# Kernel tuning notes

Measured on AMD Instinct MI355X. Metric: run time of the kernel, lower is better.

The kernel has to match this reference:

```python
import jax, jax.numpy as jnp
import numpy as np

N_QUBITS = 10
N_LAYERS = 4
NUM_CLASSES = 10
BATCH = 2048
DIM = 1 << N_QUBITS  # 1024 state-vector dimension

# basis-state bit tables (wire w <-> bit position w; any consistent ordering
# yields identical PauliZ expectation values)
_d = np.arange(DIM)
_bits = (_d[None, :] >> np.arange(N_QUBITS)[:, None]) & 1          # [n, D]
_SIGN = jnp.asarray(1.0 - 2.0 * _bits, dtype=jnp.float32)         # [n, D], z_w(d) = +/-1
_ZZ = _SIGN[:-1] * _SIGN[1:]                                       # [n-1, D], z_i*z_{i+1}
# CNOT(control=i, target=i+1) basis permutations (self-inverse)
_CNOT_PERM = [np.where((_d >> i) & 1, _d ^ (1 << (i + 1)), _d) for i in range(N_QUBITS - 1)]


def _apply_ry(state, theta, wire):
    # state: [B, D] complex64, theta: scalar angle, RY = [[c,-s],[s,c]], c=cos(theta/2)
    B, D = state.shape
    lo = 1 << wire
    st = state.reshape(B, D // (2 * lo), 2, lo)
    c = jnp.cos(0.5 * theta)
    s = jnp.sin(0.5 * theta)
    s0, s1 = st[:, :, 0, :], st[:, :, 1, :]
    return jnp.stack([c * s0 - s * s1, s * s0 + c * s1], axis=2).reshape(B, D)


def _circuit(inp, weights):
    # inp: [B, n] rotation angles (pre_net output), weights: [L+1, n]
    B = inp.shape[0]
    # Hadamards on |0...0> -> uniform superposition
    state = jnp.full((B, DIM), DIM ** -0.5, dtype=jnp.complex64)
    # ZZFeatureMap is fully diagonal: RZ(2*x_i) gives phase exp(-1j*x_i*z_i);
    # CNOT-RZ(2*(pi-x_i)*(pi-x_{i+1}))-CNOT gives phase exp(-1j*(pi-x_i)*(pi-x_{i+1})*z_i*z_{i+1})
    ang = inp @ _SIGN + ((np.pi - inp[:, :-1]) * (np.pi - inp[:, 1:])) @ _ZZ  # [B, D]
    state = state * jnp.exp(-1j * ang)
    # RealAmplitudes-style ansatz
    for l in range(N_LAYERS):
        for i in range(N_QUBITS):
            state = _apply_ry(state, weights[l, i], i)
        for p in _CNOT_PERM:
            state = state[:, p]
    for i in range(N_QUBITS):
        state = _apply_ry(state, weights[N_LAYERS, i], i)
    probs = jnp.square(state.real) + jnp.square(state.imag)  # [B, D]
    return probs @ _SIGN.T                                    # [B, n] PauliZ expvals


def setup_inputs() -> dict:
    k = jax.random.split(jax.random.key(0), 5)
    x = jax.random.normal(k[0], (BATCH, N_QUBITS), jnp.float32)
    W_pre = jax.random.normal(k[1], (N_QUBITS, N_QUBITS), jnp.float32) / np.sqrt(N_QUBITS).astype(np.float32)
    b_pre = jnp.zeros((N_QUBITS,), jnp.float32)
    # TorchLayer default init: uniform(0, 2*pi)
    weights = jax.random.uniform(k[2], (N_LAYERS + 1, N_QUBITS), jnp.float32, 0.0, 2.0 * np.pi)
    W_post = jax.random.normal(k[3], (NUM_CLASSES, N_QUBITS), jnp.float32) / np.sqrt(N_QUBITS).astype(np.float32)
    b_post = jnp.zeros((NUM_CLASSES,), jnp.float32)
    return {"x": x, "W_pre": W_pre, "b_pre": b_pre, "weights": weights,
            "W_post": W_post, "b_post": b_post}


def reference(x, W_pre, b_pre, weights, W_post, b_post):
    h = x @ W_pre.T + b_pre          # pre_net
    q = _circuit(h, weights)         # qlayer: batched state-vector simulation
    return q @ W_post.T + b_post     # post_net
```

## Files before the change

kernel.cpp:

```cpp
#include <hip/hip_runtime.h>

#define NQ   10
#define NL   4
#define NCL  10
#define PI_F 3.14159265358979f

typedef float f2 __attribute__((ext_vector_type(2)));

__device__ __forceinline__ f2 pk_mul2(f2 a, f2 b) {
    f2 d;
    asm("v_pk_mul_f32 %0, %1, %2" : "=v"(d) : "v"(a), "v"(b));
    return d;
}
__device__ __forceinline__ f2 pk_fma2(f2 a, f2 b, f2 c) {
    f2 d;
    asm("v_pk_fma_f32 %0, %1, %2, %3" : "=v"(d) : "v"(a), "v"(b), "v"(c));
    return d;
}
__device__ __forceinline__ f2 pk_add2(f2 a, f2 b) {
    f2 d;
    asm("v_pk_add_f32 %0, %1, %2" : "=v"(d) : "v"(a), "v"(b));
    return d;
}

__device__ __forceinline__ float bcastf(float v, int l) {
    return __int_as_float(__builtin_amdgcn_readlane(__float_as_int(v), l));
}

__device__ __forceinline__ float bperm(int byteaddr, float v) {
    return __int_as_float(__builtin_amdgcn_ds_bpermute(byteaddr, __float_as_int(v)));
}

template<int M>
__device__ __forceinline__ float xlane(float v) {
    if constexpr (M == 1) {
        return __int_as_float(__builtin_amdgcn_update_dpp(
            __float_as_int(v), __float_as_int(v), 0xB1, 0xF, 0xF, false));
    } else if constexpr (M == 2) {
        return __int_as_float(__builtin_amdgcn_update_dpp(
            __float_as_int(v), __float_as_int(v), 0x4E, 0xF, 0xF, false));
    } else if constexpr (M == 4) {
        return __int_as_float(__builtin_amdgcn_ds_swizzle(
            __float_as_int(v), 0x101F));
    } else if constexpr (M == 8) {
        return __int_as_float(__builtin_amdgcn_update_dpp(
            __float_as_int(v), __float_as_int(v), 0x128, 0xF, 0xF, false));
    } else if constexpr (M == 16) {
        auto r = __builtin_amdgcn_permlane16_swap(
            (unsigned)__float_as_int(v), (unsigned)__float_as_int(v), false, false);
        return __int_as_float((int)(r[0] ^ r[1] ^ (unsigned)__float_as_int(v)));
    } else {
        auto r = __builtin_amdgcn_permlane32_swap(
            (unsigned)__float_as_int(v), (unsigned)__float_as_int(v), false, false);
        return __int_as_float((int)(r[0] ^ r[1] ^ (unsigned)__float_as_int(v)));
    }
}

template<int M>
__device__ __forceinline__ f2 xlane2(f2 v) {
    f2 r; r.x = xlane<M>(v.x); r.y = xlane<M>(v.y); return r;
}

template<int M>
__device__ __forceinline__ void xwire2(float c, float s, int lane, f2 (&sc)[16]) {
    const float se = (lane & M) ? s : -s;
    const f2 c2 = {c, c}, se2 = {se, se};
    #pragma unroll
    for (int r = 0; r < 16; ++r) {
        f2 t = xlane2<M>(sc[r]);
        sc[r] = pk_fma2(se2, t, pk_mul2(c2, sc[r]));
    }
}

__device__ __forceinline__ f2 bsum2(f2 v) {
    v = pk_add2(v, xlane2<1 >(v));
    v = pk_add2(v, xlane2<2 >(v));
    v = pk_add2(v, xlane2<4 >(v));
    v = pk_add2(v, xlane2<8 >(v));
    v = pk_add2(v, xlane2<16>(v));
    v = pk_add2(v, xlane2<32>(v));
    return v;
}

__global__ __launch_bounds__(256)
void qnn_kernel(const float* __restrict__ x,
                const float* __restrict__ W_pre,
                const float* __restrict__ b_pre,
                const float* __restrict__ weights,
                const float* __restrict__ W_post,
                const float* __restrict__ b_post,
                float* __restrict__ out, int batch)
{
    const int lane = threadIdx.x & 63;
    const int b = blockIdx.x * 4 + (threadIdx.x >> 6);
    if (b >= batch) return;
    const int bu = __builtin_amdgcn_readfirstlane(b);

    float cw = 0.0f, sw = 0.0f;
    if (lane < (NL + 1) * NQ) {
        float th = 0.5f * weights[lane];
        __sincosf(th, &sw, &cw);
    }

    float xv[NQ];
    #pragma unroll
    for (int k = 0; k < NQ; ++k) xv[k] = x[bu * NQ + k];
    float h[NQ];
    #pragma unroll
    for (int j = 0; j < NQ; ++j) {
        float acc = b_pre[j];
        #pragma unroll
        for (int k = 0; k < NQ; ++k)
            acc = fmaf(xv[k], W_pre[j * NQ + k], acc);
        h[j] = acc;
    }
    float z[NQ - 1];
    #pragma unroll
    for (int i = 0; i < NQ - 1; ++i) z[i] = (PI_F - h[i]) * (PI_F - h[i + 1]);

    float A = 0.0f;
    #pragma unroll
    for (int i = 4; i < NQ; ++i)
        A += ((lane >> (i - 4)) & 1) ? -h[i] : h[i];
    #pragma unroll
    for (int i = 4; i < NQ - 1; ++i)
        A += (((lane >> (i - 4)) ^ (lane >> (i - 3))) & 1) ? -z[i] : z[i];

    f2 sc[16];
    #pragma unroll
    for (int r = 0; r < 16; ++r) {
        float ang = A;
        #pragma unroll
        for (int i = 0; i < 4; ++i)
            ang += ((r >> i) & 1) ? -h[i] : h[i];
        #pragma unroll
        for (int i = 0; i < 3; ++i)
            ang += (((r >> i) ^ (r >> (i + 1))) & 1) ? -z[i] : z[i];
        ang += (((r >> 3) ^ lane) & 1) ? -z[3] : z[3];
        float sn, cn;
        __sincosf(ang, &sn, &cn);
        sc[r].x = 0.03125f * cn;
        sc[r].y = -0.03125f * sn;
    }

    const int plbase = (lane ^ (lane << 1)) & 0x3F;
    const int paddr0 = plbase << 2;
    const int paddr1 = (plbase ^ 1) << 2;

    #pragma clang loop unroll(disable)
    for (int l = 0; l <= NL; ++l) {
        if (l > 0) {
            f2 np[16];
            #pragma unroll
            for (int r = 0; r < 16; ++r) {
                const int rp = (r ^ (r << 1)) & 0xF;
                const int pa = (r < 8) ? paddr0 : paddr1;
                np[r].x = bperm(pa, sc[rp].x);
                np[r].y = bperm(pa, sc[rp].y);
            }
            #pragma unroll
            for (int r = 0; r < 16; ++r) sc[r] = np[r];
        }

        const int base = l * NQ;

        #pragma unroll
        for (int w = 0; w < 4; ++w) {
            const float c = bcastf(cw, base + w);
            const float s = bcastf(sw, base + w);
            const f2 c2 = {c, c}, s2 = {s, s}, ns2 = {-s, -s};
            #pragma unroll
            for (int r = 0; r < 16; ++r) {
                if (r & (1 << w)) continue;
                const int q = r | (1 << w);
                f2 a0 = sc[r], a1 = sc[q];
                sc[r] = pk_fma2(ns2, a1, pk_mul2(c2, a0));
                sc[q] = pk_fma2(s2,  a0, pk_mul2(c2, a1));
            }
        }

        xwire2<1 >(bcastf(cw, base + 4), bcastf(sw, base + 4), lane, sc);
        xwire2<2 >(bcastf(cw, base + 5), bcastf(sw, base + 5), lane, sc);
        xwire2<4 >(bcastf(cw, base + 6), bcastf(sw, base + 6), lane, sc);
        xwire2<8 >(bcastf(cw, base + 7), bcastf(sw, base + 7), lane, sc);
        xwire2<16>(bcastf(cw, base + 8), bcastf(sw, base + 8), lane, sc);
        xwire2<32>(bcastf(cw, base + 9), bcastf(sw, base + 9), lane, sc);
    }

    float P = 0.0f, p0 = 0.0f, p1 = 0.0f, p2 = 0.0f, p3 = 0.0f;
    #pragma unroll
    for (int r = 0; r < 16; ++r) {
        f2 qq = pk_mul2(sc[r], sc[r]);
        float pr = qq.x + qq.y;
        P  += pr;
        p0 += (r & 1) ? -pr : pr;
        p1 += (r & 2) ? -pr : pr;
        p2 += (r & 4) ? -pr : pr;
        p3 += (r & 8) ? -pr : pr;
    }
    f2 qa = bsum2((f2){p0, p1});
    f2 qb = bsum2((f2){p2, p3});
    {
        float t;
        t = xlane<1 >(P); P = t + ((lane & 1 ) ? -P : P);
        t = xlane<2 >(P); P = t + ((lane & 2 ) ? -P : P);
        t = xlane<4 >(P); P = t + ((lane & 4 ) ? -P : P);
        t = xlane<8 >(P); P = t + ((lane & 8 ) ? -P : P);
        t = xlane<16>(P); P = t + ((lane & 16) ? -P : P);
        t = xlane<32>(P); P = t + ((lane & 32) ? -P : P);
    }
    float q[NCL];
    q[0] = qa.x; q[1] = qa.y; q[2] = qb.x; q[3] = qb.y;
    q[4] = bcastf(P, 1);
    q[5] = bcastf(P, 2);
    q[6] = bcastf(P, 4);
    q[7] = bcastf(P, 8);
    q[8] = bcastf(P, 16);
    q[9] = bcastf(P, 32);

    if (lane < NCL) {
        float o = b_post[lane];
        #pragma unroll
        for (int k = 0; k < NCL; ++k)
            o = fmaf(q[k], W_post[lane * NQ + k], o);
        out[b * NCL + lane] = o;
    }
}

extern "C" void kernel_launch(void* const* d_in, const int* in_sizes, int n_in,
                              void* d_out, int out_size, void* d_ws, size_t ws_size,
                              hipStream_t stream) {
    const float* x       = (const float*)d_in[0];
    const float* W_pre   = (const float*)d_in[1];
    const float* b_pre   = (const float*)d_in[2];
    const float* weights = (const float*)d_in[3];
    const float* W_post  = (const float*)d_in[4];
    const float* b_post  = (const float*)d_in[5];
    float* outp = (float*)d_out;
    int batch = in_sizes[0] / NQ;
    int grid = (batch + 3) / 4;
    qnn_kernel<<<grid, 256, 0, stream>>>(x, W_pre, b_pre, weights, W_post, b_post, outp, batch);
}
```

Baseline: 28.14 us.

## Split each sample's state vector across two wavefronts with LDS exchange for wire 0

Each batch sample is now simulated by a 128-thread block of two wavefronts. Each wave holds 8 amplitude pairs per lane instead of 16, with wire 0 mapped to the wave index. The wire-0 rotation exchanges halves through double-buffered shared memory with a block barrier each layer, and the final expectation values are combined across the two waves in LDS. The aim is to halve per-thread register state and double wave-level parallelism, in exchange for LDS traffic and five extra barriers per sample.

```diff
diff --git a/kernel.cpp b/kernel.cpp
--- a/kernel.cpp
+++ b/kernel.cpp
@@ -8,25 +8,18 @@
 typedef float f2 __attribute__((ext_vector_type(2)));
 
 __device__ __forceinline__ f2 pk_mul2(f2 a, f2 b) {
-    f2 d;
-    asm("v_pk_mul_f32 %0, %1, %2" : "=v"(d) : "v"(a), "v"(b));
-    return d;
+    f2 d; asm("v_pk_mul_f32 %0, %1, %2" : "=v"(d) : "v"(a), "v"(b)); return d;
 }
 __device__ __forceinline__ f2 pk_fma2(f2 a, f2 b, f2 c) {
-    f2 d;
-    asm("v_pk_fma_f32 %0, %1, %2, %3" : "=v"(d) : "v"(a), "v"(b), "v"(c));
-    return d;
+    f2 d; asm("v_pk_fma_f32 %0, %1, %2, %3" : "=v"(d) : "v"(a), "v"(b), "v"(c)); return d;
 }
 __device__ __forceinline__ f2 pk_add2(f2 a, f2 b) {
-    f2 d;
-    asm("v_pk_add_f32 %0, %1, %2" : "=v"(d) : "v"(a), "v"(b));
-    return d;
+    f2 d; asm("v_pk_add_f32 %0, %1, %2" : "=v"(d) : "v"(a), "v"(b)); return d;
 }
 
 __device__ __forceinline__ float bcastf(float v, int l) {
     return __int_as_float(__builtin_amdgcn_readlane(__float_as_int(v), l));
 }
-
 __device__ __forceinline__ float bperm(int byteaddr, float v) {
     return __int_as_float(__builtin_amdgcn_ds_bpermute(byteaddr, __float_as_int(v)));
 }
@@ -55,21 +48,20 @@
         return __int_as_float((int)(r[0] ^ r[1] ^ (unsigned)__float_as_int(v)));
     }
 }
-
 template<int M>
 __device__ __forceinline__ f2 xlane2(f2 v) {
     f2 r; r.x = xlane<M>(v.x); r.y = xlane<M>(v.y); return r;
 }
 
 template<int M>
-__device__ __forceinline__ void xwire2(float c, float s, int lane, f2 (&sc)[16]) {
+__device__ __forceinline__ void xwire8(float c, float s, int lane, f2 (&sc)[8]) {
     const float se = (lane & M) ? s : -s;
     const f2 c2 = {c, c}, se2 = {se, se};
-    #pragma unroll
-    for (int r = 0; r < 16; ++r) {
-        f2 t = xlane2<M>(sc[r]);
-        sc[r] = pk_fma2(se2, t, pk_mul2(c2, sc[r]));
-    }
+    f2 t[8];
+    #pragma unroll
+    for (int r = 0; r < 8; ++r) t[r] = xlane2<M>(sc[r]);
+    #pragma unroll
+    for (int r = 0; r < 8; ++r) sc[r] = pk_fma2(se2, t[r], pk_mul2(c2, sc[r]));
 }
 
 __device__ __forceinline__ f2 bsum2(f2 v) {
@@ -82,7 +74,7 @@
     return v;
 }
 
-__global__ __launch_bounds__(256)
+__global__ __launch_bounds__(128, 4)
 void qnn_kernel(const float* __restrict__ x,
                 const float* __restrict__ W_pre,
                 const float* __restrict__ b_pre,
@@ -91,10 +83,13 @@
                 const float* __restrict__ b_post,
                 float* __restrict__ out, int batch)
 {
-    const int lane = threadIdx.x & 63;
-    const int b = blockIdx.x * 4 + (threadIdx.x >> 6);
-    if (b >= batch) return;
-    const int bu = __builtin_amdgcn_readfirstlane(b);
+    __shared__ f2 xch[2][2][8][64];
+    __shared__ float sq[2][NCL];
+
+    const int tid  = threadIdx.x;
+    const int lane = tid & 63;
+    const int W    = tid >> 6;
+    const int b    = blockIdx.x;
 
     float cw = 0.0f, sw = 0.0f;
     if (lane < (NL + 1) * NQ) {
@@ -104,7 +99,7 @@
 
     float xv[NQ];
     #pragma unroll
-    for (int k = 0; k < NQ; ++k) xv[k] = x[bu * NQ + k];
+    for (int k = 0; k < NQ; ++k) xv[k] = x[b * NQ + k];
     float h[NQ];
     #pragma unroll
     for (int j = 0; j < NQ; ++j) {
@@ -118,59 +113,72 @@
     #pragma unroll
     for (int i = 0; i < NQ - 1; ++i) z[i] = (PI_F - h[i]) * (PI_F - h[i + 1]);
 
-    float A = 0.0f;
-    #pragma unroll
-    for (int i = 4; i < NQ; ++i)
-        A += ((lane >> (i - 4)) & 1) ? -h[i] : h[i];
-    #pragma unroll
-    for (int i = 4; i < NQ - 1; ++i)
-        A += (((lane >> (i - 4)) ^ (lane >> (i - 3))) & 1) ? -z[i] : z[i];
-
-    f2 sc[16];
-    #pragma unroll
-    for (int r = 0; r < 16; ++r) {
+    float A = W ? -h[0] : h[0];
+    #pragma unroll
+    for (int i = 0; i < 6; ++i)
+        A += ((lane >> i) & 1) ? -h[4 + i] : h[4 + i];
+    #pragma unroll
+    for (int j = 0; j < 5; ++j)
+        A += (((lane >> j) ^ (lane >> (j + 1))) & 1) ? -z[4 + j] : z[4 + j];
+    const float zw0 = W ? -z[0] : z[0];
+    const float zl3 = (lane & 1) ? -z[3] : z[3];
+
+    f2 sc[8];
+    #pragma unroll
+    for (int r = 0; r < 8; ++r) {
         float ang = A;
-        #pragma unroll
-        for (int i = 0; i < 4; ++i)
-            ang += ((r >> i) & 1) ? -h[i] : h[i];
-        #pragma unroll
-        for (int i = 0; i < 3; ++i)
-            ang += (((r >> i) ^ (r >> (i + 1))) & 1) ? -z[i] : z[i];
-        ang += (((r >> 3) ^ lane) & 1) ? -z[3] : z[3];
+        ang += (r & 1) ? -h[1] : h[1];
+        ang += (r & 2) ? -h[2] : h[2];
+        ang += (r & 4) ? -h[3] : h[3];
+        ang += (r & 1) ? -zw0 : zw0;
+        ang += ((r ^ (r >> 1)) & 1) ? -z[1] : z[1];
+        ang += (((r >> 1) ^ (r >> 2)) & 1) ? -z[2] : z[2];
+        ang += (r & 4) ? -zl3 : zl3;
         float sn, cn;
         __sincosf(ang, &sn, &cn);
         sc[r].x = 0.03125f * cn;
         sc[r].y = -0.03125f * sn;
     }
 
-    const int plbase = (lane ^ (lane << 1)) & 0x3F;
-    const int paddr0 = plbase << 2;
-    const int paddr1 = (plbase ^ 1) << 2;
+    const int plb = (lane ^ (lane << 1)) & 0x3F;
+    const int pa0 = plb << 2;
+    const int pa1 = (plb ^ 1) << 2;
+    int pp = 0;
 
     #pragma clang loop unroll(disable)
     for (int l = 0; l <= NL; ++l) {
         if (l > 0) {
-            f2 np[16];
-            #pragma unroll
-            for (int r = 0; r < 16; ++r) {
-                const int rp = (r ^ (r << 1)) & 0xF;
-                const int pa = (r < 8) ? paddr0 : paddr1;
-                np[r].x = bperm(pa, sc[rp].x);
-                np[r].y = bperm(pa, sc[rp].y);
+            f2 np[8];
+            if (W == 0) {
+                #pragma unroll
+                for (int r = 0; r < 8; ++r) {
+                    const int rp = (r ^ (r << 1)) & 7;
+                    const int pa = (r < 4) ? pa0 : pa1;
+                    np[r].x = bperm(pa, sc[rp].x);
+                    np[r].y = bperm(pa, sc[rp].y);
+                }
+            } else {
+                #pragma unroll
+                for (int r = 0; r < 8; ++r) {
+                    const int rp = ((r ^ (r << 1)) & 7) ^ 1;
+                    const int pa = (r < 4) ? pa0 : pa1;
+                    np[r].x = bperm(pa, sc[rp].x);
+                    np[r].y = bperm(pa, sc[rp].y);
+                }
             }
             #pragma unroll
-            for (int r = 0; r < 16; ++r) sc[r] = np[r];
+            for (int r = 0; r < 8; ++r) sc[r] = np[r];
         }
 
         const int base = l * NQ;
 
         #pragma unroll
-        for (int w = 0; w < 4; ++w) {
-            const float c = bcastf(cw, base + w);
-            const float s = bcastf(sw, base + w);
+        for (int w = 0; w < 3; ++w) {
+            const float c = bcastf(cw, base + 1 + w);
+            const float s = bcastf(sw, base + 1 + w);
             const f2 c2 = {c, c}, s2 = {s, s}, ns2 = {-s, -s};
             #pragma unroll
-            for (int r = 0; r < 16; ++r) {
+            for (int r = 0; r < 8; ++r) {
                 if (r & (1 << w)) continue;
                 const int q = r | (1 << w);
                 f2 a0 = sc[r], a1 = sc[q];
@@ -179,27 +187,42 @@
             }
         }
 
-        xwire2<1 >(bcastf(cw, base + 4), bcastf(sw, base + 4), lane, sc);
-        xwire2<2 >(bcastf(cw, base + 5), bcastf(sw, base + 5), lane, sc);
-        xwire2<4 >(bcastf(cw, base + 6), bcastf(sw, base + 6), lane, sc);
-        xwire2<8 >(bcastf(cw, base + 7), bcastf(sw, base + 7), lane, sc);
-        xwire2<16>(bcastf(cw, base + 8), bcastf(sw, base + 8), lane, sc);
-        xwire2<32>(bcastf(cw, base + 9), bcastf(sw, base + 9), lane, sc);
-    }
-
-    float P = 0.0f, p0 = 0.0f, p1 = 0.0f, p2 = 0.0f, p3 = 0.0f;
-    #pragma unroll
-    for (int r = 0; r < 16; ++r) {
+        xwire8<1 >(bcastf(cw, base + 4), bcastf(sw, base + 4), lane, sc);
+        xwire8<2 >(bcastf(cw, base + 5), bcastf(sw, base + 5), lane, sc);
+        xwire8<4 >(bcastf(cw, base + 6), bcastf(sw, base + 6), lane, sc);
+        xwire8<8 >(bcastf(cw, base + 7), bcastf(sw, base + 7), lane, sc);
+        xwire8<16>(bcastf(cw, base + 8), bcastf(sw, base + 8), lane, sc);
+        xwire8<32>(bcastf(cw, base + 9), bcastf(sw, base + 9), lane, sc);
+
+        {
+            const float c = bcastf(cw, base + 0);
+            const float s = bcastf(sw, base + 0);
+            #pragma unroll
+            for (int r = 0; r < 8; ++r) xch[pp][W][r][lane] = sc[r];
+            __syncthreads();
+            const float se = W ? s : -s;
+            const f2 c2 = {c, c}, se2 = {se, se};
+            #pragma unroll
+            for (int r = 0; r < 8; ++r) {
+                f2 t = xch[pp][W ^ 1][r][lane];
+                sc[r] = pk_fma2(se2, t, pk_mul2(c2, sc[r]));
+            }
+            pp ^= 1;
+        }
+    }
+
+    float P = 0.0f, p0 = 0.0f, p1 = 0.0f, p2 = 0.0f;
+    #pragma unroll
+    for (int r = 0; r < 8; ++r) {
         f2 qq = pk_mul2(sc[r], sc[r]);
         float pr = qq.x + qq.y;
         P  += pr;
         p0 += (r & 1) ? -pr : pr;
         p1 += (r & 2) ? -pr : pr;
         p2 += (r & 4) ? -pr : pr;
-        p3 += (r & 8) ? -pr : pr;
     }
     f2 qa = bsum2((f2){p0, p1});
-    f2 qb = bsum2((f2){p2, p3});
+    f2 qb = bsum2((f2){p2, p2});
     {
         float t;
         t = xlane<1 >(P); P = t + ((lane & 1 ) ? -P : P);
@@ -209,20 +232,23 @@
         t = xlane<16>(P); P = t + ((lane & 16) ? -P : P);
         t = xlane<32>(P); P = t + ((lane & 32) ? -P : P);
     }
-    float q[NCL];
-    q[0] = qa.x; q[1] = qa.y; q[2] = qb.x; q[3] = qb.y;
-    q[4] = bcastf(P, 1);
-    q[5] = bcastf(P, 2);
-    q[6] = bcastf(P, 4);
-    q[7] = bcastf(P, 8);
-    q[8] = bcastf(P, 16);
-    q[9] = bcastf(P, 32);
-
-    if (lane < NCL) {
+    const float T  = bcastf(P, 0);
+    const float s4 = bcastf(P, 1),  s5 = bcastf(P, 2),  s6 = bcastf(P, 4);
+    const float s7 = bcastf(P, 8),  s8 = bcastf(P, 16), s9 = bcastf(P, 32);
+
+    if (lane == 0) {
+        sq[W][0] = W ? -T : T;
+        sq[W][1] = qa.x; sq[W][2] = qa.y; sq[W][3] = qb.x;
+        sq[W][4] = s4; sq[W][5] = s5; sq[W][6] = s6;
+        sq[W][7] = s7; sq[W][8] = s8; sq[W][9] = s9;
+    }
+    __syncthreads();
+
+    if (W == 0 && lane < NCL) {
         float o = b_post[lane];
         #pragma unroll
         for (int k = 0; k < NCL; ++k)
-            o = fmaf(q[k], W_post[lane * NQ + k], o);
+            o = fmaf(sq[0][k] + sq[1][k], W_post[lane * NQ + k], o);
         out[b * NCL + lane] = o;
     }
 }
@@ -238,6 +264,5 @@
     const float* b_post  = (const float*)d_in[5];
     float* outp = (float*)d_out;
     int batch = in_sizes[0] / NQ;
-    int grid = (batch + 3) / 4;
-    qnn_kernel<<<grid, 256, 0, stream>>>(x, W_pre, b_pre, weights, W_post, b_post, outp, batch);
-}
+    qnn_kernel<<<batch, 128, 0, stream>>>(x, W_pre, b_pre, weights, W_post, b_post, outp, batch);
+}
```

Measured after the change: 30.34 us. 7.8% more time.

## Launch one wavefront per block and batch cross-lane swaps before FMAs

Applied to the files above, without the earlier changes.

Switches the launch to one 64-thread block per sample instead of four wavefronts per 256-thread block, and drops the bounds check and readfirstlane. Restructures the cross-lane wire updates so all 16 lane exchanges are issued before the FMAs, which exposes more independent exchanges to hide their latency but raises register pressure. Replaces the XOR trick that extracts the partner value from permlane swaps with a compare-and-select.

```diff
diff --git a/kernel.cpp b/kernel.cpp
--- a/kernel.cpp
+++ b/kernel.cpp
@@ -8,25 +8,18 @@
 typedef float f2 __attribute__((ext_vector_type(2)));
 
 __device__ __forceinline__ f2 pk_mul2(f2 a, f2 b) {
-    f2 d;
-    asm("v_pk_mul_f32 %0, %1, %2" : "=v"(d) : "v"(a), "v"(b));
-    return d;
+    f2 d; asm("v_pk_mul_f32 %0, %1, %2" : "=v"(d) : "v"(a), "v"(b)); return d;
 }
 __device__ __forceinline__ f2 pk_fma2(f2 a, f2 b, f2 c) {
-    f2 d;
-    asm("v_pk_fma_f32 %0, %1, %2, %3" : "=v"(d) : "v"(a), "v"(b), "v"(c));
-    return d;
+    f2 d; asm("v_pk_fma_f32 %0, %1, %2, %3" : "=v"(d) : "v"(a), "v"(b), "v"(c)); return d;
 }
 __device__ __forceinline__ f2 pk_add2(f2 a, f2 b) {
-    f2 d;
-    asm("v_pk_add_f32 %0, %1, %2" : "=v"(d) : "v"(a), "v"(b));
-    return d;
+    f2 d; asm("v_pk_add_f32 %0, %1, %2" : "=v"(d) : "v"(a), "v"(b)); return d;
 }
 
 __device__ __forceinline__ float bcastf(float v, int l) {
     return __int_as_float(__builtin_amdgcn_readlane(__float_as_int(v), l));
 }
-
 __device__ __forceinline__ float bperm(int byteaddr, float v) {
     return __int_as_float(__builtin_amdgcn_ds_bpermute(byteaddr, __float_as_int(v)));
 }
@@ -46,16 +39,17 @@
         return __int_as_float(__builtin_amdgcn_update_dpp(
             __float_as_int(v), __float_as_int(v), 0x128, 0xF, 0xF, false));
     } else if constexpr (M == 16) {
-        auto r = __builtin_amdgcn_permlane16_swap(
-            (unsigned)__float_as_int(v), (unsigned)__float_as_int(v), false, false);
-        return __int_as_float((int)(r[0] ^ r[1] ^ (unsigned)__float_as_int(v)));
+        unsigned own = (unsigned)__float_as_int(v);
+        auto r = __builtin_amdgcn_permlane16_swap(own, own, false, false);
+        unsigned p = (r[0] == own) ? (unsigned)r[1] : (unsigned)r[0];
+        return __int_as_float((int)p);
     } else {
-        auto r = __builtin_amdgcn_permlane32_swap(
-            (unsigned)__float_as_int(v), (unsigned)__float_as_int(v), false, false);
-        return __int_as_float((int)(r[0] ^ r[1] ^ (unsigned)__float_as_int(v)));
-    }
-}
-
+        unsigned own = (unsigned)__float_as_int(v);
+        auto r = __builtin_amdgcn_permlane32_swap(own, own, false, false);
+        unsigned p = (r[0] == own) ? (unsigned)r[1] : (unsigned)r[0];
+        return __int_as_float((int)p);
+    }
+}
 template<int M>
 __device__ __forceinline__ f2 xlane2(f2 v) {
     f2 r; r.x = xlane<M>(v.x); r.y = xlane<M>(v.y); return r;
@@ -65,11 +59,11 @@
 __device__ __forceinline__ void xwire2(float c, float s, int lane, f2 (&sc)[16]) {
     const float se = (lane & M) ? s : -s;
     const f2 c2 = {c, c}, se2 = {se, se};
-    #pragma unroll
-    for (int r = 0; r < 16; ++r) {
-        f2 t = xlane2<M>(sc[r]);
-        sc[r] = pk_fma2(se2, t, pk_mul2(c2, sc[r]));
-    }
+    f2 t[16];
+    #pragma unroll
+    for (int r = 0; r < 16; ++r) t[r] = xlane2<M>(sc[r]);
+    #pragma unroll
+    for (int r = 0; r < 16; ++r) sc[r] = pk_fma2(se2, t[r], pk_mul2(c2, sc[r]));
 }
 
 __device__ __forceinline__ f2 bsum2(f2 v) {
@@ -82,7 +76,7 @@
     return v;
 }
 
-__global__ __launch_bounds__(256)
+__global__ __launch_bounds__(64)
 void qnn_kernel(const float* __restrict__ x,
                 const float* __restrict__ W_pre,
                 const float* __restrict__ b_pre,
@@ -91,10 +85,8 @@
                 const float* __restrict__ b_post,
                 float* __restrict__ out, int batch)
 {
-    const int lane = threadIdx.x & 63;
-    const int b = blockIdx.x * 4 + (threadIdx.x >> 6);
-    if (b >= batch) return;
-    const int bu = __builtin_amdgcn_readfirstlane(b);
+    const int lane = threadIdx.x;
+    const int b = blockIdx.x;
 
     float cw = 0.0f, sw = 0.0f;
     if (lane < (NL + 1) * NQ) {
@@ -104,7 +96,7 @@
 
     float xv[NQ];
     #pragma unroll
-    for (int k = 0; k < NQ; ++k) xv[k] = x[bu * NQ + k];
+    for (int k = 0; k < NQ; ++k) xv[k] = x[b * NQ + k];
     float h[NQ];
     #pragma unroll
     for (int j = 0; j < NQ; ++j) {
@@ -238,6 +230,5 @@
     const float* b_post  = (const float*)d_in[5];
     float* outp = (float*)d_out;
     int batch = in_sizes[0] / NQ;
-    int grid = (batch + 3) / 4;
-    qnn_kernel<<<grid, 256, 0, stream>>>(x, W_pre, b_pre, weights, W_post, b_post, outp, batch);
-}
+    qnn_kernel<<<batch, 64, 0, stream>>>(x, W_pre, b_pre, weights, W_post, b_post, outp, batch);
+}
```

Result: no change. 28.09 us (-0.2%).
